# Kernel optimization log

Measured on AMD Instinct MI355X. Metric: run time of the kernel, lower is better.

The kernel has to match this reference:

```python
import jax, jax.numpy as jnp
import numpy as np

HIDDEN, NHEAD, NLAYERS = 128, 8, 4
N, H, W = 1, 36, 192


def _layernorm(x, w, b, eps=1e-5):
    mu = x.mean(-1, keepdims=True)
    var = ((x - mu) ** 2).mean(-1, keepdims=True)
    return (x - mu) * jax.lax.rsqrt(var + eps) * w + b


def _mha_rel(q_in, k_in, v_in, in_w, in_b, out_w, out_b, pos_sel, attn_mask):
    # q_in/k_in/v_in: [w, bsz, C]; pos_sel: [w, w, C] (already gathered by pos_indexes)
    w, bsz, C = q_in.shape
    hd = C // NHEAD
    scale = float(hd) ** -0.5
    wq, wk, wv = in_w[:C], in_w[C:2 * C], in_w[2 * C:]
    bq, bk, bv = in_b[:C], in_b[C:2 * C], in_b[2 * C:]
    q = (q_in @ wq.T + bq) * scale
    k = k_in @ wk.T + bk
    v = v_in @ wv.T + bv
    q_r = (pos_sel @ wq.T + bq) * scale            # [w,w,C]
    k_r = pos_sel @ wk.T + bk                       # [w,w,C]
    q = q.reshape(w, bsz, NHEAD, hd)
    k = k.reshape(w, bsz, NHEAD, hd)
    v = v.reshape(w, bsz, NHEAD, hd)
    q_r = q_r.reshape(w, w, NHEAD, hd)
    k_r = k_r.reshape(w, w, NHEAD, hd)
    # content-content + content-pos + pos-content -> [bsz, heads, w, w]
    attn = (jnp.einsum('wnec,vnec->newv', q, k)
            + jnp.einsum('wnec,wvec->newv', q, k_r)
            + jnp.einsum('vnec,wvec->newv', k, q_r))
    if attn_mask is not None:
        attn = attn + attn_mask[None, None]
    raw = attn
    a = jax.nn.softmax(attn, axis=-1)
    vo = jnp.einsum('newv,vnec->wnec', a, v).reshape(w, bsz, C)
    vo = vo @ out_w.T + out_b
    return vo, raw.sum(axis=1)  # raw summed over heads, [bsz,w,w]


def setup_inputs():
    key = jax.random.key(0)
    ks = jax.random.split(key, 8)
    C, L = HIDDEN, NLAYERS
    s = 0.02
    rn = lambda k, shape, sc: jax.random.normal(k, shape, dtype=jnp.float32) * sc
    return dict(
        feat_left=rn(ks[0], (N, C, H, W), 1.0),
        feat_right=rn(ks[1], (N, C, H, W), 1.0),
        pos_enc=rn(ks[2], (2 * W - 1, C), 1.0),
        sa_in_w=rn(ks[3], (L, 3 * C, C), s),
        sa_in_b=jnp.zeros((L, 3 * C), jnp.float32),
        sa_out_w=rn(ks[4], (L, C, C), s),
        sa_out_b=jnp.zeros((L, C), jnp.float32),
        sa_ln_w=jnp.ones((L, C), jnp.float32),
        sa_ln_b=jnp.zeros((L, C), jnp.float32),
        ca_in_w=rn(ks[5], (L, 3 * C, C), s),
        ca_in_b=jnp.zeros((L, 3 * C), jnp.float32),
        ca_out_w=rn(ks[6], (L, C, C), s),
        ca_out_b=jnp.zeros((L, C), jnp.float32),
        ca_ln1_w=jnp.ones((L, C), jnp.float32),
        ca_ln1_b=jnp.zeros((L, C), jnp.float32),
        ca_ln2_w=jnp.ones((L, C), jnp.float32),
        ca_ln2_b=jnp.zeros((L, C), jnp.float32),
    )


def reference(feat_left, feat_right, pos_enc,
              sa_in_w, sa_in_b, sa_out_w, sa_out_b, sa_ln_w, sa_ln_b,
              ca_in_w, ca_in_b, ca_out_w, ca_out_b,
              ca_ln1_w, ca_ln1_b, ca_ln2_w, ca_ln2_b):
    n, C, h, w = feat_left.shape
    hn = h * n
    # [N,C,H,W] -> [W,HN,C]
    fl = jnp.transpose(feat_left, (3, 2, 0, 1)).reshape(w, hn, C)
    fr = jnp.transpose(feat_right, (3, 2, 0, 1)).reshape(w, hn, C)
    # relative position indexes: (w-1..0) col + (0..w-1) row, flattened
    idx = (np.arange(w - 1, -1, -1)[:, None] + np.arange(w)[None, :]).reshape(-1)
    pos_sel = pos_enc[idx].reshape(w, w, C)             # for left-query attention
    pos_sel_flip = pos_enc[::-1][idx].reshape(w, w, C)  # flipped pos for right-query
    causal_mask = jnp.triu(jnp.full((w, w), -jnp.inf, dtype=jnp.float32), k=1)

    feat = jnp.concatenate([fl, fr], axis=1)  # [W, 2HN, C]
    raw_last = None
    for i in range(NLAYERS):
        # ---- self attention on concatenated tokens ----
        f2 = _layernorm(feat, sa_ln_w[i], sa_ln_b[i])
        vo, _ = _mha_rel(f2, f2, f2, sa_in_w[i], sa_in_b[i], sa_out_w[i], sa_out_b[i],
                         pos_sel, None)
        feat = feat + vo
        # ---- cross attention (shared weights for both directions) ----
        left, right = feat[:, :hn], feat[:, hn:]
        l2 = _layernorm(left, ca_ln1_w[i], ca_ln1_b[i])
        r2 = _layernorm(right, ca_ln1_w[i], ca_ln1_b[i])
        vo, _ = _mha_rel(r2, l2, l2, ca_in_w[i], ca_in_b[i], ca_out_w[i], ca_out_b[i],
                         pos_sel_flip, None)
        right = right + vo
        mask = causal_mask if i == NLAYERS - 1 else None
        r2b = _layernorm(right, ca_ln2_w[i], ca_ln2_b[i])
        vo, raw = _mha_rel(l2, r2b, r2b, ca_in_w[i], ca_in_b[i], ca_out_w[i], ca_out_b[i],
                           pos_sel, mask)
        left = left + vo
        feat = jnp.concatenate([left, right], axis=1)
        raw_last = raw
    # raw_last: [HN, W, W] -> [N, H, W, W]
    attn_weight = raw_last.reshape(h, n, w, w).transpose(1, 0, 2, 3)
    return attn_weight, feat
```

## Files before the change

kernel.cpp:

```cpp
#include <hip/hip_runtime.h>
#include <cmath>

#define W 192
#define CC 128
#define BSA 72
#define BCA 36
#define TSA (W*BSA)
#define TCA (W*BCA)
#define CH 32
#define SLD 200

__global__ __launch_bounds__(256) void pack_feat_k(const float* __restrict__ fl,
                                                   const float* __restrict__ fr,
                                                   float* __restrict__ feat) {
  __shared__ float tile[32][33];
  int b = blockIdx.z;
  const float* src = (b < BCA) ? fl : fr;
  int h = (b < BCA) ? b : b - BCA;
  int w0 = blockIdx.x * 32, c0 = blockIdx.y * 32;
  int tx = threadIdx.x & 31, ty = threadIdx.x >> 5;
#pragma unroll
  for (int rr = 0; rr < 4; ++rr) {
    int c = ty + rr * 8;
    tile[c][tx] = src[((c0 + c) * BCA + h) * W + w0 + tx];
  }
  __syncthreads();
#pragma unroll
  for (int rr = 0; rr < 4; ++rr) {
    int wl = ty + rr * 8;
    feat[(((w0 + wl) * BSA) + b) * CC + c0 + tx] = tile[tx][wl];
  }
}

template<int TM, int LNMODE>
__device__ __forceinline__ void gemm_core(
    const float* __restrict__ A, int lda, int aob, int aooff,
    const float* __restrict__ lnw, const float* __restrict__ lnb,
    const float* __restrict__ Bw, int ldb,
    const float* __restrict__ bias,
    float* __restrict__ C, float* __restrict__ Cb, int ldc,
    int M, int N, int noff, int scale_abs, int accum, int ob, int ooff) {
  constexpr int MR = TM / 16;
  constexpr int AS = TM + 4;
  __shared__ float AsT[32 * AS];
  __shared__ float BsT[32 * 132];
  int tid = threadIdx.x;
  int ty = tid >> 4, tx = tid & 15;
  int t0 = blockIdx.x * TM, n0 = blockIdx.y * 128;
  int row_l = tid >> 3, qk7 = tid & 7;
  float acc[MR][8] = {};

  float4 va[(LNMODE == 1) ? TM / 32 : 1][4];
  float mu2[TM / 32], rs2[TM / 32];
  if constexpr (LNMODE == 1) {
    float4 gv[4], bvv[4];
#pragma unroll
    for (int c4 = 0; c4 < 4; ++c4) {
      gv[c4]  = *reinterpret_cast<const float4*>(lnw + c4 * 32 + qk7 * 4);
      bvv[c4] = *reinterpret_cast<const float4*>(lnb + c4 * 32 + qk7 * 4);
    }
#pragma unroll
    for (int p = 0; p < TM / 32; ++p) {
      int ar = t0 + row_l + p * 32;
      if (ar >= M) ar = M - 1;
      int sr = (ar / aob) * BSA + (ar % aob) + aooff;
      const float* arow = A + (long)sr * lda;
      float sum = 0.f, sq = 0.f;
#pragma unroll
      for (int c4 = 0; c4 < 4; ++c4) {
        va[p][c4] = *reinterpret_cast<const float4*>(arow + c4 * 32 + qk7 * 4);
        sum += va[p][c4].x + va[p][c4].y + va[p][c4].z + va[p][c4].w;
        sq += va[p][c4].x * va[p][c4].x + va[p][c4].y * va[p][c4].y
            + va[p][c4].z * va[p][c4].z + va[p][c4].w * va[p][c4].w;
      }
      sum += __shfl_xor(sum, 1); sum += __shfl_xor(sum, 2); sum += __shfl_xor(sum, 4);
      sq  += __shfl_xor(sq, 1);  sq  += __shfl_xor(sq, 2);  sq  += __shfl_xor(sq, 4);
      float mu = sum * (1.f / 128.f);
      float var = sq * (1.f / 128.f) - mu * mu;
      float rstd = 1.0f / sqrtf(var + 1e-5f);
#pragma unroll
      for (int c4 = 0; c4 < 4; ++c4) {
        va[p][c4].x = (va[p][c4].x - mu) * rstd * gv[c4].x + bvv[c4].x;
        va[p][c4].y = (va[p][c4].y - mu) * rstd * gv[c4].y + bvv[c4].y;
        va[p][c4].z = (va[p][c4].z - mu) * rstd * gv[c4].z + bvv[c4].z;
        va[p][c4].w = (va[p][c4].w - mu) * rstd * gv[c4].w + bvv[c4].w;
      }
    }
  } else if constexpr (LNMODE == 2) {
#pragma unroll
    for (int p = 0; p < TM / 32; ++p) {
      int ar = t0 + row_l + p * 32;
      if (ar >= M) ar = M - 1;
      int sr = (ar / aob) * BSA + (ar % aob) + aooff;
      const float* arow = A + (long)sr * lda;
      float sum = 0.f, sq = 0.f;
#pragma unroll
      for (int c4 = 0; c4 < 4; ++c4) {
        float4 v = *reinterpret_cast<const float4*>(arow + c4 * 32 + qk7 * 4);
        sum += v.x + v.y + v.z + v.w;
        sq += v.x * v.x + v.y * v.y + v.z * v.z + v.w * v.w;
      }
      sum += __shfl_xor(sum, 1); sum += __shfl_xor(sum, 2); sum += __shfl_xor(sum, 4);
      sq  += __shfl_xor(sq, 1);  sq  += __shfl_xor(sq, 2);  sq  += __shfl_xor(sq, 4);
      float mu = sum * (1.f / 128.f);
      float var = sq * (1.f / 128.f) - mu * mu;
      mu2[p] = mu;
      rs2[p] = 1.0f / sqrtf(var + 1e-5f);
    }
  }

  for (int kcc = 0; kcc < 4; ++kcc) {
    int kc = kcc * 32;
#pragma unroll
    for (int p = 0; p < TM / 32; ++p) {
      int row = row_l + p * 32;
      float4 av;
      if constexpr (LNMODE == 1) {
        av = va[p][kcc];
      } else if constexpr (LNMODE == 2) {
        int ar = t0 + row;
        if (ar >= M) ar = M - 1;
        int sr = (ar / aob) * BSA + (ar % aob) + aooff;
        av = *reinterpret_cast<const float4*>(A + (long)sr * lda + kc + qk7 * 4);
        float4 gq = *reinterpret_cast<const float4*>(lnw + kc + qk7 * 4);
        float4 bq = *reinterpret_cast<const float4*>(lnb + kc + qk7 * 4);
        av.x = (av.x - mu2[p]) * rs2[p] * gq.x + bq.x;
        av.y = (av.y - mu2[p]) * rs2[p] * gq.y + bq.y;
        av.z = (av.z - mu2[p]) * rs2[p] * gq.z + bq.z;
        av.w = (av.w - mu2[p]) * rs2[p] * gq.w + bq.w;
      } else {
        int arow = t0 + row;
        av = make_float4(0.f, 0.f, 0.f, 0.f);
        if (arow < M) av = *reinterpret_cast<const float4*>(A + (long)arow * lda + kc + qk7 * 4);
      }
      AsT[(qk7 * 4 + 0) * AS + row] = av.x;
      AsT[(qk7 * 4 + 1) * AS + row] = av.y;
      AsT[(qk7 * 4 + 2) * AS + row] = av.z;
      AsT[(qk7 * 4 + 3) * AS + row] = av.w;
    }
#pragma unroll
    for (int p = 0; p < 4; ++p) {
      int id = tid + p * 256;
      int row = id >> 3, qk = id & 7;
      int brow = n0 + row;
      float4 bv = make_float4(0.f, 0.f, 0.f, 0.f);
      if (brow < N) bv = *reinterpret_cast<const float4*>(Bw + (long)brow * ldb + kc + qk * 4);
      BsT[(qk * 4 + 0) * 132 + row] = bv.x;
      BsT[(qk * 4 + 1) * 132 + row] = bv.y;
      BsT[(qk * 4 + 2) * 132 + row] = bv.z;
      BsT[(qk * 4 + 3) * 132 + row] = bv.w;
    }
    __syncthreads();
#pragma unroll
    for (int k = 0; k < 32; ++k) {
      float a[MR];
      if constexpr (MR == 2) {
        float2 a0 = *reinterpret_cast<const float2*>(&AsT[k * AS + ty * 2]);
        a[0] = a0.x; a[1] = a0.y;
      } else if constexpr (MR == 4) {
        float4 a0 = *reinterpret_cast<const float4*>(&AsT[k * AS + ty * 4]);
        a[0] = a0.x; a[1] = a0.y; a[2] = a0.z; a[3] = a0.w;
      } else {
        float4 a0 = *reinterpret_cast<const float4*>(&AsT[k * AS + ty * 8]);
        float4 a1 = *reinterpret_cast<const float4*>(&AsT[k * AS + ty * 8 + 4]);
        a[0] = a0.x; a[1] = a0.y; a[2] = a0.z; a[3] = a0.w;
        a[4] = a1.x; a[5] = a1.y; a[6] = a1.z; a[7] = a1.w;
      }
      float4 b0 = *reinterpret_cast<const float4*>(&BsT[k * 132 + tx * 8]);
      float4 b1 = *reinterpret_cast<const float4*>(&BsT[k * 132 + tx * 8 + 4]);
      float bb[8] = {b0.x, b0.y, b0.z, b0.w, b1.x, b1.y, b1.z, b1.w};
#pragma unroll
      for (int i2 = 0; i2 < MR; ++i2)
#pragma unroll
        for (int j2 = 0; j2 < 8; ++j2)
          acc[i2][j2] += a[i2] * bb[j2];
    }
    __syncthreads();
  }
#pragma unroll
  for (int i2 = 0; i2 < MR; ++i2) {
    int t = t0 + ty * MR + i2;
    if (t >= M) continue;
    int orow = ob ? ((t / ob) * BSA + (t % ob) + ooff) : t;
    float* crow = C + (long)orow * ldc + noff;
    float* crow2 = Cb ? Cb + (long)orow * ldc + noff : nullptr;
#pragma unroll
    for (int j2 = 0; j2 < 8; ++j2) {
      int n = n0 + tx * 8 + j2;
      if (n >= N) continue;
      float val = acc[i2][j2] + (bias ? bias[n] : 0.f);
      if (noff + n < scale_abs) val *= 0.25f;
      if (accum) val += crow[n];
      crow[n] = val;
      if (crow2) crow2[n] = val;
    }
  }
}

template<int TM>
__global__ __launch_bounds__(256) void gemm_g(
    const float* __restrict__ A, int lda, long abatch,
    const float* __restrict__ Bw, int ldb, long bbatch,
    const float* __restrict__ bias, int bzoff,
    float* __restrict__ C, float* __restrict__ Cb, int ldc, long cbatch,
    int M, int N, int noff, int nzoff, int scale_abs, int accum, int ob, int ooff) {
  int z = blockIdx.z;
  gemm_core<TM, 0>(A + z * abatch, lda, 1, 0, nullptr, nullptr,
                   Bw + z * bbatch, ldb,
                   bias ? bias + z * bzoff : nullptr,
                   C + z * cbatch, Cb, ldc, M, N, noff + z * nzoff,
                   scale_abs, accum, ob, ooff);
}

__global__ __launch_bounds__(256) void sa_qkv_k(
    const float* __restrict__ feat,
    const float* __restrict__ lnw, const float* __restrict__ lnb,
    const float* __restrict__ w3, const float* __restrict__ b3,
    float* __restrict__ out) {
  int z = blockIdx.z;
  gemm_core<128, 2>(feat, 128, 72, 0, lnw, lnb,
                    w3 + z * 16384, 128, b3 + z * 128,
                    out, nullptr, 384, TSA, 128, z * 128, 128, 0, 0, 0);
}

__global__ __launch_bounds__(256) void ca_qkv_k(
    const float* __restrict__ feat,
    const float* __restrict__ lnwA, const float* __restrict__ lnbA, int ooffA,
    const float* __restrict__ lnwB, const float* __restrict__ lnbB, int ooffB,
    const float* __restrict__ w3, const float* __restrict__ b3,
    float* __restrict__ out) {
  int z = blockIdx.z;
  const float* lw = (z == 0) ? lnwA : lnwB;
  const float* lb = (z == 0) ? lnbA : lnbB;
  int aoo = (z == 0) ? ooffA : ooffB;
  gemm_core<64, 1>(feat, 128, 36, aoo, lw, lb,
                   w3 + z * 16384, 128, b3 + z * 128,
                   out, nullptr, 384, TCA, 128, z * 128, 128, 0, 0, 0);
}

__global__ __launch_bounds__(256) void pos_all_k(
    const float* __restrict__ pos,
    const float* __restrict__ saw, const float* __restrict__ sab,
    const float* __restrict__ caw, const float* __restrict__ cab,
    float* __restrict__ out) {
  int z = blockIdx.z;
  int layer = z >> 2, kind = z & 3;
  const float* w = ((kind < 2) ? saw : caw) + layer * 49152 + (kind & 1) * 16384;
  const float* b = ((kind < 2) ? sab : cab) + layer * 384 + (kind & 1) * 128;
  int sc = (kind & 1) ? 0 : 128;
  gemm_core<32, 0>(pos, 128, 1, 0, nullptr, nullptr, w, 128, b,
                   out + (long)z * 49152, nullptr, 128,
                   383, 128, 0, sc, 0, 0, 0);
}

__global__ __launch_bounds__(384) void attn_k(const float* __restrict__ qkv,
                                              const float* __restrict__ qpos,
                                              const float* __restrict__ kpos,
                                              float* __restrict__ vo,
                                              int B, int flip, int domask) {
  __shared__ float q_s[CH * 20];
  __shared__ float v_s[192 * 17];
  __shared__ float u_s[2 * 223 * 20];
  __shared__ float part[384];
  __shared__ float red_m[CH], red_il[CH];
  float* kp_s = u_s;
  float* qp_s = u_s + 223 * 20;
  float* S = u_s;

  int t = threadIdx.x;
  int col = (t >= 192) ? t - 192 : t;
  int rbase = (t >= 192) ? 16 : 0;
  int b = blockIdx.z, e = blockIdx.y, w0 = blockIdx.x * CH;

  for (int idx = t; idx < 192 * 4; idx += 384) {
    int row = idx >> 2, q4 = idx & 3;
    float4 kv = *reinterpret_cast<const float4*>(qkv + ((long)row * B + b) * 384 + 128 + e * 16 + q4 * 4);
    v_s[row * 17 + q4 * 4 + 0] = kv.x; v_s[row * 17 + q4 * 4 + 1] = kv.y;
    v_s[row * 17 + q4 * 4 + 2] = kv.z; v_s[row * 17 + q4 * 4 + 3] = kv.w;
  }
  __syncthreads();
  float kr[16];
#pragma unroll
  for (int d = 0; d < 16; ++d) kr[d] = v_s[col * 17 + d];
  __syncthreads();
  for (int idx = t; idx < 192 * 4; idx += 384) {
    int row = idx >> 2, q4 = idx & 3;
    float4 vv = *reinterpret_cast<const float4*>(qkv + ((long)row * B + b) * 384 + 256 + e * 16 + q4 * 4);
    v_s[row * 17 + q4 * 4 + 0] = vv.x; v_s[row * 17 + q4 * 4 + 1] = vv.y;
    v_s[row * 17 + q4 * 4 + 2] = vv.z; v_s[row * 17 + q4 * 4 + 3] = vv.w;
  }
  if (t < CH * 4) {
    int row = t >> 2, q4 = t & 3;
    float4 qv = *reinterpret_cast<const float4*>(qkv + ((long)(w0 + row) * B + b) * 384 + e * 16 + q4 * 4);
    *reinterpret_cast<float4*>(q_s + row * 20 + q4 * 4) = qv;
  }
  int base = flip ? w0 : (191 - (w0 + CH - 1));
  for (int idx = t; idx < 223 * 4; idx += 384) {
    int row = idx >> 2, q4 = idx & 3;
    int gidx = base + row;
    float4 kpv = make_float4(0.f, 0.f, 0.f, 0.f), qpv = kpv;
    if (gidx >= 0 && gidx < 383) {
      kpv = *reinterpret_cast<const float4*>(kpos + (long)gidx * 128 + e * 16 + q4 * 4);
      qpv = *reinterpret_cast<const float4*>(qpos + (long)gidx * 128 + e * 16 + q4 * 4);
    }
    *reinterpret_cast<float4*>(kp_s + row * 20 + q4 * 4) = kpv;
    *reinterpret_cast<float4*>(qp_s + row * 20 + q4 * 4) = qpv;
  }
  __syncthreads();

  float s[16];
#pragma unroll
  for (int rr = 0; rr < 16; ++rr) {
    int r = rbase + rr;
    int j = flip ? (191 + r - col) : (CH - 1 - r + col);
    const float4* kp4 = reinterpret_cast<const float4*>(kp_s + j * 20);
    const float4* qp4 = reinterpret_cast<const float4*>(qp_s + j * 20);
    const float4* qq4 = reinterpret_cast<const float4*>(q_s + r * 20);
    float acc = 0.f;
#pragma unroll
    for (int d4 = 0; d4 < 4; ++d4) {
      float4 kp = kp4[d4], qp = qp4[d4], qq = qq4[d4];
      acc += qq.x * (kr[d4 * 4 + 0] + kp.x) + kr[d4 * 4 + 0] * qp.x;
      acc += qq.y * (kr[d4 * 4 + 1] + kp.y) + kr[d4 * 4 + 1] * qp.y;
      acc += qq.z * (kr[d4 * 4 + 2] + kp.z) + kr[d4 * 4 + 2] * qp.z;
      acc += qq.w * (kr[d4 * 4 + 3] + kp.w) + kr[d4 * 4 + 3] * qp.w;
    }
    s[rr] = (domask && col > w0 + r) ? -INFINITY : acc;
  }
  __syncthreads();

#pragma unroll
  for (int rr = 0; rr < 16; ++rr) S[(rbase + rr) * SLD + col] = s[rr];
  __syncthreads();

  int r12 = t / 12, tr = t - r12 * 12;
  float4 xx[4];
  {
    float mloc = -INFINITY;
#pragma unroll
    for (int q = 0; q < 4; ++q) {
      xx[q] = *reinterpret_cast<const float4*>(S + r12 * SLD + tr * 16 + q * 4);
      mloc = fmaxf(mloc, fmaxf(fmaxf(xx[q].x, xx[q].y), fmaxf(xx[q].z, xx[q].w)));
    }
    part[t] = mloc;
  }
  __syncthreads();
  if (t < CH) {
    float m = part[t * 12];
#pragma unroll
    for (int i = 1; i < 12; ++i) m = fmaxf(m, part[t * 12 + i]);
    red_m[t] = m;
  }
  __syncthreads();
  {
    float m = red_m[r12];
    float lloc = 0.f;
#pragma unroll
    for (int q = 0; q < 4; ++q) {
      xx[q].x = __expf(xx[q].x - m);
      xx[q].y = __expf(xx[q].y - m);
      xx[q].z = __expf(xx[q].z - m);
      xx[q].w = __expf(xx[q].w - m);
      lloc += xx[q].x + xx[q].y + xx[q].z + xx[q].w;
      *reinterpret_cast<float4*>(S + r12 * SLD + tr * 16 + q * 4) = xx[q];
    }
    part[t] = lloc;
  }
  __syncthreads();
  if (t < CH) {
    float l = 0.f;
#pragma unroll
    for (int i = 0; i < 12; ++i) l += part[t * 12 + i];
    red_il[t] = 1.0f / l;
  }
  __syncthreads();

  int d = t & 15, g = t >> 4;
  int r0 = g, r1 = g + 24;
  float a0 = 0.f, a1 = 0.f;
#pragma unroll 8
  for (int v4 = 0; v4 < 48; ++v4) {
    float4 s0 = *reinterpret_cast<const float4*>(S + r0 * SLD + v4 * 4);
    float va = v_s[(v4 * 4 + 0) * 17 + d];
    float vb = v_s[(v4 * 4 + 1) * 17 + d];
    float vc = v_s[(v4 * 4 + 2) * 17 + d];
    float vd = v_s[(v4 * 4 + 3) * 17 + d];
    a0 += s0.x * va + s0.y * vb + s0.z * vc + s0.w * vd;
    if (g < 8) {
      float4 s1 = *reinterpret_cast<const float4*>(S + r1 * SLD + v4 * 4);
      a1 += s1.x * va + s1.y * vb + s1.z * vc + s1.w * vd;
    }
  }
  vo[((long)(w0 + r0) * B + b) * 128 + e * 16 + d] = a0 * red_il[r0];
  if (g < 8)
    vo[((long)(w0 + r1) * B + b) * 128 + e * 16 + d] = a1 * red_il[r1];
}

__global__ __launch_bounds__(256) void gather_k(const float* __restrict__ D,
                                                const float* __restrict__ E,
                                                float* __restrict__ out) {
  __shared__ float E_s[192][33];
  int b = blockIdx.y, w0 = blockIdx.x * 32;
  for (int idx = threadIdx.x; idx < 192 * 32; idx += 256) {
    int v = idx >> 5, j = idx & 31;
    int u = 160 + v - w0 + j;
    E_s[v][j] = (u >= 0 && u < 192) ? E[((long)v * BCA + b) * 192 + u] : 0.f;
  }
  __syncthreads();
  int lane = threadIdx.x & 63, wl = threadIdx.x >> 6;
#pragma unroll
  for (int i = 0; i < 8; ++i) {
    int w = w0 + wl * 8 + i;
    int j = w0 + 31 - w;
#pragma unroll
    for (int kv = 0; kv < 3; ++kv) {
      int v = lane + kv * 64;
      long o = ((long)b * W + w) * W + v;
      if (v > w) {
        out[o] = -1e30f;
      } else {
        out[o] = out[o] + D[((long)w * BCA + b) * 192 + 191 + v - w] + E_s[v][j];
      }
    }
  }
}

extern "C" void kernel_launch(void* const* d_in, const int* in_sizes, int n_in,
                              void* d_out, int out_size, void* d_ws, size_t ws_size,
                              hipStream_t stream) {
  (void)in_sizes; (void)n_in; (void)out_size; (void)ws_size;
  const float* feat_left  = (const float*)d_in[0];
  const float* feat_right = (const float*)d_in[1];
  const float* pos_enc    = (const float*)d_in[2];
  const float* sa_in_w    = (const float*)d_in[3];
  const float* sa_in_b    = (const float*)d_in[4];
  const float* sa_out_w   = (const float*)d_in[5];
  const float* sa_out_b   = (const float*)d_in[6];
  const float* sa_ln_w    = (const float*)d_in[7];
  const float* sa_ln_b    = (const float*)d_in[8];
  const float* ca_in_w    = (const float*)d_in[9];
  const float* ca_in_b    = (const float*)d_in[10];
  const float* ca_out_w   = (const float*)d_in[11];
  const float* ca_out_b   = (const float*)d_in[12];
  const float* ca_ln1_w   = (const float*)d_in[13];
  const float* ca_ln1_b   = (const float*)d_in[14];
  const float* ca_ln2_w   = (const float*)d_in[15];
  const float* ca_ln2_b   = (const float*)d_in[16];

  float* ws   = (float*)d_ws;
  float* feat = ws;
  float* qkv  = feat + 1769472;
  float* vo   = qkv + 5308416;
  float* posA = vo + 1769472;
  float* Dbuf = qkv + 2654208;
  float* Ebuf = Dbuf + 1327104;

  float* raw_out  = (float*)d_out;
  float* feat_out = raw_out + 1327104;

  pack_feat_k<<<dim3(6, 4, 72), 256, 0, stream>>>(feat_left, feat_right, feat);
  pos_all_k<<<dim3(12, 1, 16), 256, 0, stream>>>(pos_enc, sa_in_w, sa_in_b, ca_in_w, ca_in_b, posA);

  for (int i = 0; i < 4; ++i) {
    const float* inw  = sa_in_w + i * 49152;
    const float* inb  = sa_in_b + i * 384;
    const float* outw = sa_out_w + i * 16384;
    const float* outb = sa_out_b + i * 128;
    const float* saQ = posA + (long)(i * 4 + 0) * 49152;
    const float* saK = posA + (long)(i * 4 + 1) * 49152;
    const float* caQ = posA + (long)(i * 4 + 2) * 49152;
    const float* caK = posA + (long)(i * 4 + 3) * 49152;
    const float* ln1w = ca_ln1_w + i * 128, *ln1b = ca_ln1_b + i * 128;
    const float* ln2w = ca_ln2_w + i * 128, *ln2b = ca_ln2_b + i * 128;
    float* fo = (i == 3) ? feat_out : nullptr;

    sa_qkv_k<<<dim3(108, 1, 3), 256, 0, stream>>>(feat, sa_ln_w + i * 128, sa_ln_b + i * 128, inw, inb, qkv);
    attn_k<<<dim3(6, 8, 72), 384, 0, stream>>>(qkv, saQ, saK, vo, 72, 0, 0);
    gemm_g<64><<<dim3(216, 1, 1), 256, 0, stream>>>(vo, 128, 0, outw, 128, 0, outb, 0,
                                                    feat, nullptr, 128, 0, TSA, 128, 0, 0, 0, 1, 0, 0);

    const float* cinw  = ca_in_w + i * 49152;
    const float* cinb  = ca_in_b + i * 384;
    const float* coutw = ca_out_w + i * 16384;
    const float* coutb = ca_out_b + i * 128;
    ca_qkv_k<<<dim3(108, 1, 3), 256, 0, stream>>>(feat, ln1w, ln1b, 36, ln1w, ln1b, 0, cinw, cinb, qkv);
    attn_k<<<dim3(6, 8, 36), 384, 0, stream>>>(qkv, caQ, caK, vo, 36, 1, 0);
    gemm_g<32><<<dim3(216, 1, 1), 256, 0, stream>>>(vo, 128, 0, coutw, 128, 0, coutb, 0,
                                                    feat, fo, 128, 0, TCA, 128, 0, 0, 0, 1, 36, 36);
    ca_qkv_k<<<dim3(108, 1, 3), 256, 0, stream>>>(feat, ln1w, ln1b, 0, ln2w, ln2b, 36, cinw, cinb, qkv);
    attn_k<<<dim3(6, 8, 36), 384, 0, stream>>>(qkv, caQ, caK, vo, 36, 0, (i == 3) ? 1 : 0);
    if (i == 3) {
      gemm_g<64><<<dim3(108, 2, 2), 256, 0, stream>>>(qkv, 384, 128, caK, 128, -49152, nullptr, 0,
                                                      Dbuf, nullptr, 192, 1327104, TCA, 192, 0, 0, 0, 0, 0, 0);
      gemm_g<32><<<dim3(6, 2, 36), 256, 0, stream>>>(qkv, 13824, 384, qkv + 128, 13824, 384, nullptr, 0,
                                                     raw_out, nullptr, 192, 36864, 192, 192, 0, 0, 0, 0, 0, 0);
      gather_k<<<dim3(6, 36), 256, 0, stream>>>(Dbuf, Ebuf, raw_out);
    }
    gemm_g<32><<<dim3(216, 1, 1), 256, 0, stream>>>(vo, 128, 0, coutw, 128, 0, coutb, 0,
                                                    feat, fo, 128, 0, TCA, 128, 0, 0, 0, 1, 36, 0);
  }
}
```

Measured before the change: 1.707 ms.

## Shrink GEMM row tiles, drop LN mode 2, transpose V in attention shared memory

The self-attention QKV GEMM moves from a 128-row tile with a two-pass layernorm (mode 2) to 64-row tiles with register-held normalized rows (mode 1), and the mode-2 path is removed. The out-projection and the final D GEMM also use smaller row tiles with doubled grids. In the attention kernel, V is stored transposed in shared memory so the PV loop reads one float4 per step instead of four strided scalars, and K staging reuses the u_s buffer, which shrinks the shared-memory footprint. The smaller tiles raise block count and occupancy at the cost of reloading weights more often per row.

Measured after the change: 1.595 ms. 1.07x faster.

```diff
diff --git a/kernel.cpp b/kernel.cpp
--- a/kernel.cpp
+++ b/kernel.cpp
@@ -51,7 +51,6 @@
   float acc[MR][8] = {};
 
   float4 va[(LNMODE == 1) ? TM / 32 : 1][4];
-  float mu2[TM / 32], rs2[TM / 32];
   if constexpr (LNMODE == 1) {
     float4 gv[4], bvv[4];
 #pragma unroll
@@ -86,27 +85,6 @@
         va[p][c4].w = (va[p][c4].w - mu) * rstd * gv[c4].w + bvv[c4].w;
       }
     }
-  } else if constexpr (LNMODE == 2) {
-#pragma unroll
-    for (int p = 0; p < TM / 32; ++p) {
-      int ar = t0 + row_l + p * 32;
-      if (ar >= M) ar = M - 1;
-      int sr = (ar / aob) * BSA + (ar % aob) + aooff;
-      const float* arow = A + (long)sr * lda;
-      float sum = 0.f, sq = 0.f;
-#pragma unroll
-      for (int c4 = 0; c4 < 4; ++c4) {
-        float4 v = *reinterpret_cast<const float4*>(arow + c4 * 32 + qk7 * 4);
-        sum += v.x + v.y + v.z + v.w;
-        sq += v.x * v.x + v.y * v.y + v.z * v.z + v.w * v.w;
-      }
-      sum += __shfl_xor(sum, 1); sum += __shfl_xor(sum, 2); sum += __shfl_xor(sum, 4);
-      sq  += __shfl_xor(sq, 1);  sq  += __shfl_xor(sq, 2);  sq  += __shfl_xor(sq, 4);
-      float mu = sum * (1.f / 128.f);
-      float var = sq * (1.f / 128.f) - mu * mu;
-      mu2[p] = mu;
-      rs2[p] = 1.0f / sqrtf(var + 1e-5f);
-    }
   }
 
   for (int kcc = 0; kcc < 4; ++kcc) {
@@ -117,17 +95,6 @@
       float4 av;
       if constexpr (LNMODE == 1) {
         av = va[p][kcc];
-      } else if constexpr (LNMODE == 2) {
-        int ar = t0 + row;
-        if (ar >= M) ar = M - 1;
-        int sr = (ar / aob) * BSA + (ar % aob) + aooff;
-        av = *reinterpret_cast<const float4*>(A + (long)sr * lda + kc + qk7 * 4);
-        float4 gq = *reinterpret_cast<const float4*>(lnw + kc + qk7 * 4);
-        float4 bq = *reinterpret_cast<const float4*>(lnb + kc + qk7 * 4);
-        av.x = (av.x - mu2[p]) * rs2[p] * gq.x + bq.x;
-        av.y = (av.y - mu2[p]) * rs2[p] * gq.y + bq.y;
-        av.z = (av.z - mu2[p]) * rs2[p] * gq.z + bq.z;
-        av.w = (av.w - mu2[p]) * rs2[p] * gq.w + bq.w;
       } else {
         int arow = t0 + row;
         av = make_float4(0.f, 0.f, 0.f, 0.f);
@@ -218,9 +185,9 @@
     const float* __restrict__ w3, const float* __restrict__ b3,
     float* __restrict__ out) {
   int z = blockIdx.z;
-  gemm_core<128, 2>(feat, 128, 72, 0, lnw, lnb,
-                    w3 + z * 16384, 128, b3 + z * 128,
-                    out, nullptr, 384, TSA, 128, z * 128, 128, 0, 0, 0);
+  gemm_core<64, 1>(feat, 128, 72, 0, lnw, lnb,
+                   w3 + z * 16384, 128, b3 + z * 128,
+                   out, nullptr, 384, TSA, 128, z * 128, 128, 0, 0, 0);
 }
 
 __global__ __launch_bounds__(256) void ca_qkv_k(
@@ -259,7 +226,7 @@
                                               float* __restrict__ vo,
                                               int B, int flip, int domask) {
   __shared__ float q_s[CH * 20];
-  __shared__ float v_s[192 * 17];
+  __shared__ float vT[16 * 196];
   __shared__ float u_s[2 * 223 * 20];
   __shared__ float part[384];
   __shared__ float red_m[CH], red_il[CH];
@@ -275,19 +242,21 @@
   for (int idx = t; idx < 192 * 4; idx += 384) {
     int row = idx >> 2, q4 = idx & 3;
     float4 kv = *reinterpret_cast<const float4*>(qkv + ((long)row * B + b) * 384 + 128 + e * 16 + q4 * 4);
-    v_s[row * 17 + q4 * 4 + 0] = kv.x; v_s[row * 17 + q4 * 4 + 1] = kv.y;
-    v_s[row * 17 + q4 * 4 + 2] = kv.z; v_s[row * 17 + q4 * 4 + 3] = kv.w;
+    u_s[row * 17 + q4 * 4 + 0] = kv.x; u_s[row * 17 + q4 * 4 + 1] = kv.y;
+    u_s[row * 17 + q4 * 4 + 2] = kv.z; u_s[row * 17 + q4 * 4 + 3] = kv.w;
   }
   __syncthreads();
   float kr[16];
 #pragma unroll
-  for (int d = 0; d < 16; ++d) kr[d] = v_s[col * 17 + d];
+  for (int d = 0; d < 16; ++d) kr[d] = u_s[col * 17 + d];
   __syncthreads();
   for (int idx = t; idx < 192 * 4; idx += 384) {
     int row = idx >> 2, q4 = idx & 3;
     float4 vv = *reinterpret_cast<const float4*>(qkv + ((long)row * B + b) * 384 + 256 + e * 16 + q4 * 4);
-    v_s[row * 17 + q4 * 4 + 0] = vv.x; v_s[row * 17 + q4 * 4 + 1] = vv.y;
-    v_s[row * 17 + q4 * 4 + 2] = vv.z; v_s[row * 17 + q4 * 4 + 3] = vv.w;
+    vT[(q4 * 4 + 0) * 196 + row] = vv.x;
+    vT[(q4 * 4 + 1) * 196 + row] = vv.y;
+    vT[(q4 * 4 + 2) * 196 + row] = vv.z;
+    vT[(q4 * 4 + 3) * 196 + row] = vv.w;
   }
   if (t < CH * 4) {
     int row = t >> 2, q4 = t & 3;
@@ -380,15 +349,12 @@
   float a0 = 0.f, a1 = 0.f;
 #pragma unroll 8
   for (int v4 = 0; v4 < 48; ++v4) {
+    float4 vv = *reinterpret_cast<const float4*>(vT + d * 196 + v4 * 4);
     float4 s0 = *reinterpret_cast<const float4*>(S + r0 * SLD + v4 * 4);
-    float va = v_s[(v4 * 4 + 0) * 17 + d];
-    float vb = v_s[(v4 * 4 + 1) * 17 + d];
-    float vc = v_s[(v4 * 4 + 2) * 17 + d];
-    float vd = v_s[(v4 * 4 + 3) * 17 + d];
-    a0 += s0.x * va + s0.y * vb + s0.z * vc + s0.w * vd;
+    a0 += s0.x * vv.x + s0.y * vv.y + s0.z * vv.z + s0.w * vv.w;
     if (g < 8) {
       float4 s1 = *reinterpret_cast<const float4*>(S + r1 * SLD + v4 * 4);
-      a1 += s1.x * va + s1.y * vb + s1.z * vc + s1.w * vd;
+      a1 += s1.x * vv.x + s1.y * vv.y + s1.z * vv.z + s1.w * vv.w;
     }
   }
   vo[((long)(w0 + r0) * B + b) * 128 + e * 16 + d] = a0 * red_il[r0];
@@ -474,9 +440,9 @@
     const float* ln2w = ca_ln2_w + i * 128, *ln2b = ca_ln2_b + i * 128;
     float* fo = (i == 3) ? feat_out : nullptr;
 
-    sa_qkv_k<<<dim3(108, 1, 3), 256, 0, stream>>>(feat, sa_ln_w + i * 128, sa_ln_b + i * 128, inw, inb, qkv);
+    sa_qkv_k<<<dim3(216, 1, 3), 256, 0, stream>>>(feat, sa_ln_w + i * 128, sa_ln_b + i * 128, inw, inb, qkv);
     attn_k<<<dim3(6, 8, 72), 384, 0, stream>>>(qkv, saQ, saK, vo, 72, 0, 0);
-    gemm_g<64><<<dim3(216, 1, 1), 256, 0, stream>>>(vo, 128, 0, outw, 128, 0, outb, 0,
+    gemm_g<32><<<dim3(432, 1, 1), 256, 0, stream>>>(vo, 128, 0, outw, 128, 0, outb, 0,
                                                     feat, nullptr, 128, 0, TSA, 128, 0, 0, 0, 1, 0, 0);
 
     const float* cinw  = ca_in_w + i * 49152;
@@ -490,7 +456,7 @@
     ca_qkv_k<<<dim3(108, 1, 3), 256, 0, stream>>>(feat, ln1w, ln1b, 0, ln2w, ln2b, 36, cinw, cinb, qkv);
     attn_k<<<dim3(6, 8, 36), 384, 0, stream>>>(qkv, caQ, caK, vo, 36, 0, (i == 3) ? 1 : 0);
     if (i == 3) {
-      gemm_g<64><<<dim3(108, 2, 2), 256, 0, stream>>>(qkv, 384, 128, caK, 128, -49152, nullptr, 0,
+      gemm_g<32><<<dim3(216, 2, 2), 256, 0, stream>>>(qkv, 384, 128, caK, 128, -49152, nullptr, 0,
                                                       Dbuf, nullptr, 192, 1327104, TCA, 192, 0, 0, 0, 0, 0, 0);
       gemm_g<32><<<dim3(6, 2, 36), 256, 0, stream>>>(qkv, 13824, 384, qkv + 128, 13824, 384, nullptr, 0,
                                                      raw_out, nullptr, 192, 36864, 192, 192, 0, 0, 0, 0, 0, 0);
```
